# Kernel tuning notes

Hardware: AMD Instinct MI355X
Metric: run time of the kernel (lower is better)

Reference implementation:

```python
import jax, jax.numpy as jnp
import numpy as np

NUM_HEADS = 8
NUM_POINTS = 4


def _grid_sample_bilinear(img, grid, H, W):
    """torch F.grid_sample(mode='bilinear', padding='zeros', align_corners=False).
    img:  [B, H, W, D]   grid: [B, S, 2] with (x, y) in [-1, 1].
    Returns [B, S, D].
    """
    gx, gy = grid[..., 0], grid[..., 1]
    # align_corners=False pixel mapping
    x = ((gx + 1.0) * W - 1.0) * 0.5
    y = ((gy + 1.0) * H - 1.0) * 0.5
    x0 = jnp.floor(x)
    y0 = jnp.floor(y)
    wx1 = x - x0
    wy1 = y - y0
    x0i = x0.astype(jnp.int32)
    y0i = y0.astype(jnp.int32)
    img_flat = img.reshape(img.shape[0], H * W, img.shape[-1])  # [B, N, D]

    def corner(xi, yi, w):
        valid = (xi >= 0) & (xi < W) & (yi >= 0) & (yi < H)  # zeros padding
        idx = jnp.clip(yi, 0, H - 1) * W + jnp.clip(xi, 0, W - 1)  # [B, S]
        v = jnp.take_along_axis(img_flat, idx[..., None], axis=1)  # [B, S, D]
        return v * (w * valid.astype(img.dtype))[..., None]

    out = corner(x0i, y0i, (1.0 - wx1) * (1.0 - wy1))
    out += corner(x0i + 1, y0i, wx1 * (1.0 - wy1))
    out += corner(x0i, y0i + 1, (1.0 - wx1) * wy1)
    out += corner(x0i + 1, y0i + 1, wx1 * wy1)
    return out


def setup_inputs() -> dict:
    key = jax.random.key(0)
    ks = jax.random.split(key, 12)
    B, Q, D = 4, 1024, 256
    H, W = 128, 128
    nh, npts = NUM_HEADS, NUM_POINTS
    f32 = jnp.float32
    return {
        "query": jax.random.normal(ks[0], (B, Q, D), f32),
        "reference_points": jax.random.uniform(ks[1], (B, Q, 2), f32),
        "value": jax.random.normal(ks[2], (B, H * W, D), f32),
        "W_off": jax.random.normal(ks[3], (D, nh * npts * 2), f32) * 0.02,
        "b_off": jax.random.normal(ks[4], (nh * npts * 2,), f32) * 0.02,
        "W_attn": jax.random.normal(ks[5], (D, nh * npts), f32) * 0.02,
        "b_attn": jax.random.normal(ks[6], (nh * npts,), f32) * 0.02,
        "W_v": jax.random.normal(ks[7], (D, D), f32) * (D ** -0.5),
        "b_v": jnp.zeros((D,), f32),
        "W_out": jax.random.normal(ks[8], (nh * D, D), f32) * ((nh * D) ** -0.5),
        "b_out": jnp.zeros((D,), f32),
        "H": H,
        "W": W,
    }


def reference(query, reference_points, value, W_off, b_off, W_attn, b_attn,
              W_v, b_v, W_out, b_out, H, W):
    B, Q, D = query.shape
    nh, npts = NUM_HEADS, NUM_POINTS
    # learned offsets and per-point attention weights
    offsets = (query @ W_off + b_off).reshape(B, Q, nh, npts, 2)
    attn = jax.nn.softmax((query @ W_attn + b_attn).reshape(B, Q, nh, npts), axis=-1)
    # sampling locations in [-1, 1]
    locs = reference_points[:, :, None, None, :] + offsets * 0.1
    locs = jnp.clip(locs, 0.0, 1.0) * 2.0 - 1.0
    # value projection -> 2D feature map [B, H, W, D]
    img = (value @ W_v + b_v).reshape(B, H, W, D)
    # sample all heads/points at once
    grid = locs.reshape(B, Q * nh * npts, 2)
    sampled = _grid_sample_bilinear(img, grid, H, W).reshape(B, Q, nh, npts, D)
    # weighted reduce over points, concat heads
    weighted = jnp.einsum("bqhpd,bqhp->bqhd", sampled, attn)
    out = weighted.reshape(B, Q, nh * D) @ W_out + b_out
    return out
```

## Files before the change

kernel.cpp:

```cpp
#include <hip/hip_runtime.h>
#include <hip/hip_bf16.h>
#include <math.h>

constexpr int B  = 4;
constexpr int Q  = 1024;
constexpr int D  = 256;
constexpr int NH = 8;
constexpr int NP = 4;
constexpr int H  = 128;
constexpr int W  = 128;
constexpr int HW = H * W;
constexpr int KAUG = 2112;

typedef short   bf16x8  __attribute__((ext_vector_type(8)));
typedef float   f32x4   __attribute__((ext_vector_type(4)));
typedef short   short4v __attribute__((ext_vector_type(4)));
typedef unsigned short ushort8v __attribute__((ext_vector_type(8)));

__device__ inline unsigned short f2bf(float f) {
    union { float f; unsigned u; } v; v.f = f;
    unsigned r = v.u + 0x7fff + ((v.u >> 16) & 1);
    return (unsigned short)(r >> 16);
}
__device__ inline float bf2f(unsigned short s) {
    union { unsigned u; float f; } v; v.u = ((unsigned)s) << 16;
    return v.f;
}

__device__ inline void async16(const void* g, void* l) {
    __builtin_amdgcn_global_load_lds(
        (const __attribute__((address_space(1))) unsigned*)g,
        (__attribute__((address_space(3))) unsigned*)l, 16, 0, 0);
}

constexpr int R1_SG   = 0;
constexpr int R1_WC   = R1_SG + 128;
constexpr int R1_BV   = R1_WC + 128;
constexpr int R1_CONV = R1_BV + (D * 64) / 256;
constexpr int R1_END  = R1_CONV + (B * HW * D) / 4096;

__global__ __launch_bounds__(256)
void k_stage1(const float* __restrict__ value,
              const float* __restrict__ query,
              const float* __restrict__ W_off,  const float* __restrict__ b_off,
              const float* __restrict__ W_attn, const float* __restrict__ b_attn,
              const float* __restrict__ b_v,    const float* __restrict__ W_out,
              const float* __restrict__ W_v,
              unsigned short* __restrict__ val_bf,
              float* __restrict__ raw,
              unsigned short* __restrict__ WcT) {
    __shared__ __align__(16) unsigned char smemraw[16384];
    const int blk = blockIdx.x;
    const int tid = threadIdx.x;

    if (blk < R1_WC) {
        const int m0 = (blk >> 1) * 64;
        const int n0 = (blk & 1) * 64;
        float (*As)[68] = (float (*)[68])smemraw;
        float (*Bs)[68] = As + 16;
        const int tx = tid & 15, ty = tid >> 4;
        const int arow = tid >> 2, akg = (tid & 3) * 4;
        const int brow = tid >> 4, bcol = (tid & 15) * 4;

        float acc[4][4] = {};
        for (int k0 = 0; k0 < D; k0 += 16) {
            const float4 av = *(const float4*)&query[(size_t)(m0 + arow) * D + k0 + akg];
            const int kr = k0 + brow;
            const int j  = n0 + bcol;
            float4 bv;
            if (j < 64)      bv = *(const float4*)&W_off[kr * 64 + j];
            else if (j < 96) bv = *(const float4*)&W_attn[kr * 32 + (j - 64)];
            else             bv = (float4){0.f, 0.f, 0.f, 0.f};
            __syncthreads();
            As[akg + 0][arow] = av.x;
            As[akg + 1][arow] = av.y;
            As[akg + 2][arow] = av.z;
            As[akg + 3][arow] = av.w;
            *(float4*)&Bs[brow][bcol] = bv;
            __syncthreads();
            #pragma unroll
            for (int kk = 0; kk < 16; ++kk) {
                const float4 a = *(const float4*)&As[kk][ty * 4];
                const float4 b = *(const float4*)&Bs[kk][tx * 4];
                acc[0][0] += a.x * b.x; acc[0][1] += a.x * b.y; acc[0][2] += a.x * b.z; acc[0][3] += a.x * b.w;
                acc[1][0] += a.y * b.x; acc[1][1] += a.y * b.y; acc[1][2] += a.y * b.z; acc[1][3] += a.y * b.w;
                acc[2][0] += a.z * b.x; acc[2][1] += a.z * b.y; acc[2][2] += a.z * b.z; acc[2][3] += a.z * b.w;
                acc[3][0] += a.w * b.x; acc[3][1] += a.w * b.y; acc[3][2] += a.w * b.z; acc[3][3] += a.w * b.w;
            }
        }
        float bb[4];
        #pragma unroll
        for (int c = 0; c < 4; ++c) {
            const int col = n0 + tx * 4 + c;
            bb[c] = (col < 64) ? b_off[col] : ((col < 96) ? b_attn[col - 64] : 0.0f);
        }
        #pragma unroll
        for (int i = 0; i < 4; ++i) {
            const int m = m0 + ty * 4 + i;
            float4 r;
            r.x = acc[i][0] + bb[0];
            r.y = acc[i][1] + bb[1];
            r.z = acc[i][2] + bb[2];
            r.w = acc[i][3] + bb[3];
            *(float4*)&raw[(size_t)m * 128 + n0 + tx * 4] = r;
        }
    } else if (blk < R1_BV) {
        const int blkr = blk - R1_WC;
        const int z  = blkr >> 4;
        const int m0 = ((blkr >> 2) & 3) * 64;
        const int n0 = (blkr & 3) * 64;
        unsigned short* As = (unsigned short*)smemraw;
        unsigned short* Bs = As + 4096;
        const int lane = tid & 63;
        const int w    = tid >> 6;
        const int wm   = w >> 1, wn = w & 1;

        int aoff[2][2], boff[2][2];
        #pragma unroll
        for (int i = 0; i < 2; ++i)
            #pragma unroll
            for (int kk = 0; kk < 2; ++kk) {
                const int ar = wm * 32 + i * 16 + (lane & 15);
                aoff[i][kk] = ar * 64 + ((((lane >> 4) + kk * 4) ^ (ar & 7)) * 8);
                const int br = wn * 32 + i * 16 + (lane & 15);
                boff[i][kk] = br * 64 + ((((lane >> 4) + kk * 4) ^ (br & 7)) * 8);
            }

        f32x4 acc[2][2];
        #pragma unroll
        for (int i = 0; i < 2; ++i)
            #pragma unroll
            for (int j = 0; j < 2; ++j) acc[i][j] = (f32x4){0.f, 0.f, 0.f, 0.f};

        for (int it = 0; it < 4; ++it) {
            const int k0 = it * 64;
            __syncthreads();
            #pragma unroll
            for (int s = 0; s < 2; ++s) {
                const int cc = tid + s * 256;
                const int r = cc >> 3, c = cc & 7;
                const float4 v0 = *(const float4*)&W_v[(size_t)(m0 + r) * D + k0 + c * 8];
                const float4 v1 = *(const float4*)&W_v[(size_t)(m0 + r) * D + k0 + c * 8 + 4];
                ushort8v o;
                o[0] = f2bf(v0.x); o[1] = f2bf(v0.y); o[2] = f2bf(v0.z); o[3] = f2bf(v0.w);
                o[4] = f2bf(v1.x); o[5] = f2bf(v1.y); o[6] = f2bf(v1.z); o[7] = f2bf(v1.w);
                *(ushort8v*)&As[r * 64 + ((c ^ (r & 7)) * 8)] = o;
            }
            {
                const int n = tid & 63, kseg = tid >> 6;
                float vj[16];
                #pragma unroll
                for (int j = 0; j < 16; ++j)
                    vj[j] = W_out[(size_t)(z * 256 + k0 + kseg * 16 + j) * D + n0 + n];
                #pragma unroll
                for (int jj = 0; jj < 2; ++jj) {
                    ushort8v o;
                    #pragma unroll
                    for (int q = 0; q < 8; ++q) o[q] = f2bf(vj[jj * 8 + q]);
                    const int c = kseg * 2 + jj;
                    *(ushort8v*)&Bs[n * 64 + ((c ^ (n & 7)) * 8)] = o;
                }
            }
            __syncthreads();
            bf16x8 af[2][2], bfv[2][2];
            #pragma unroll
            for (int i = 0; i < 2; ++i)
                #pragma unroll
                for (int kk = 0; kk < 2; ++kk) {
                    af[i][kk]  = *(const bf16x8*)&As[aoff[i][kk]];
                    bfv[i][kk] = *(const bf16x8*)&Bs[boff[i][kk]];
                }
            #pragma unroll
            for (int i = 0; i < 2; ++i)
                #pragma unroll
                for (int j = 0; j < 2; ++j)
                    #pragma unroll
                    for (int kk = 0; kk < 2; ++kk)
                        acc[i][j] = __builtin_amdgcn_mfma_f32_16x16x32_bf16(
                            af[i][kk], bfv[j][kk], acc[i][j], 0, 0, 0);
        }

        const int colb = n0 + wn * 32 + (lane & 15);
        const int rowb = m0 + wm * 32 + (lane >> 4) * 4;
        const int ocol = z * 256;
        #pragma unroll
        for (int j = 0; j < 2; ++j) {
            const int col = colb + j * 16;
            #pragma unroll
            for (int i = 0; i < 2; ++i)
                #pragma unroll
                for (int r = 0; r < 4; ++r)
                    WcT[(size_t)col * KAUG + ocol + rowb + i * 16 + r] =
                        f2bf(acc[i][j][r]);
        }
    } else if (blk < R1_CONV) {
        const int t = (blk - R1_BV) * 256 + tid;
        const int n = t >> 6, c = t & 63;
        float v = 0.0f;
        if (c < 8) {
            #pragma unroll 8
            for (int j = 0; j < D; ++j)
                v += b_v[j] * W_out[((size_t)c * D + j) * D + n];
        }
        WcT[(size_t)n * KAUG + 2048 + c] = f2bf(v);
    } else {
        const int base = (blk - R1_CONV) * 4096;
        #pragma unroll
        for (int s = 0; s < 4; ++s) {
            const int i = base + s * 1024 + tid * 4;
            const float4 v = *(const float4*)&value[i];
            short4v o;
            o.x = (short)f2bf(v.x); o.y = (short)f2bf(v.y);
            o.z = (short)f2bf(v.z); o.w = (short)f2bf(v.w);
            *(short4v*)&val_bf[i] = o;
        }
    }
}

__global__ __launch_bounds__(256)
void k_stage2(const unsigned short* __restrict__ val,
              const float* __restrict__ raw,
              const float* __restrict__ refpts,
              unsigned short* __restrict__ sv) {
    const int bq   = blockIdx.x;
    const int b    = bq >> 10;
    const int tid  = threadIdx.x;
    const int lane = tid & 63;
    const int w    = tid >> 6;

    __shared__ float s_raw[128];
    __shared__ int   s_off[128];
    __shared__ float s_wgt[128];

    if (tid < 128) s_raw[tid] = raw[(size_t)bq * 128 + tid];
    __syncthreads();

    if (tid < NH * NP) {
        const int h = tid >> 2;
        float m = -1e30f;
        #pragma unroll
        for (int p = 0; p < NP; ++p) m = fmaxf(m, s_raw[64 + h * 4 + p]);
        float s = 0.0f;
        #pragma unroll
        for (int p = 0; p < NP; ++p) s += __expf(s_raw[64 + h * 4 + p] - m);
        const float a = __expf(s_raw[64 + tid] - m) / s;

        const float refx = refpts[(size_t)bq * 2 + 0];
        const float refy = refpts[(size_t)bq * 2 + 1];
        const float gx = fminf(fmaxf(refx + s_raw[tid * 2 + 0] * 0.1f, 0.0f), 1.0f) * 2.0f - 1.0f;
        const float gy = fminf(fmaxf(refy + s_raw[tid * 2 + 1] * 0.1f, 0.0f), 1.0f) * 2.0f - 1.0f;
        const float x  = ((gx + 1.0f) * (float)W - 1.0f) * 0.5f;
        const float y  = ((gy + 1.0f) * (float)H - 1.0f) * 0.5f;
        const float x0f = floorf(x), y0f = floorf(y);
        const float wx1 = x - x0f,  wy1 = y - y0f;
        const float wx0 = 1.0f - wx1, wy0 = 1.0f - wy1;
        const int x0 = (int)x0f, y0 = (int)y0f;
        const int x1 = x0 + 1,  y1 = y0 + 1;
        const float vx0 = (x0 >= 0 && x0 < W) ? 1.0f : 0.0f;
        const float vx1 = (x1 >= 0 && x1 < W) ? 1.0f : 0.0f;
        const float vy0 = (y0 >= 0 && y0 < H) ? 1.0f : 0.0f;
        const float vy1 = (y1 >= 0 && y1 < H) ? 1.0f : 0.0f;
        const int xc0 = min(max(x0, 0), W - 1);
        const int xc1 = min(max(x1, 0), W - 1);
        const int yc0 = min(max(y0, 0), H - 1);
        const int yc1 = min(max(y1, 0), H - 1);
        s_off[tid * 4 + 0] = yc0 * W + xc0;
        s_off[tid * 4 + 1] = yc0 * W + xc1;
        s_off[tid * 4 + 2] = yc1 * W + xc0;
        s_off[tid * 4 + 3] = yc1 * W + xc1;
        s_wgt[tid * 4 + 0] = a * wx0 * wy0 * vx0 * vy0;
        s_wgt[tid * 4 + 1] = a * wx1 * wy0 * vx1 * vy0;
        s_wgt[tid * 4 + 2] = a * wx0 * wy1 * vx0 * vy1;
        s_wgt[tid * 4 + 3] = a * wx1 * wy1 * vx1 * vy1;
    }
    __syncthreads();

    if (tid < 8) {
        float S = 0.0f;
        #pragma unroll
        for (int c = 0; c < 16; ++c) S += s_wgt[tid * 16 + c];
        sv[(size_t)bq * KAUG + 2048 + tid] = f2bf(S);
    } else if (tid < 64) {
        sv[(size_t)bq * KAUG + 2048 + tid] = 0;
    }

    const int half = lane >> 5;
    const int l5   = lane & 31;
    const unsigned short* ib = val + (size_t)b * HW * D + l5 * 8;

    ushort8v vb[16];
    float    wg[16];
    #pragma unroll
    for (int j = 0; j < 16; ++j) {
        const int flat = w * 32 + j * 2 + half;
        wg[j] = s_wgt[flat];
        vb[j] = *(const ushort8v*)(ib + (size_t)s_off[flat] * D);
    }

    float acc[2][8] = {};
    #pragma unroll
    for (int j = 0; j < 16; ++j) {
        const int g = j >> 3;
        #pragma unroll
        for (int k = 0; k < 8; ++k)
            acc[g][k] += wg[j] * bf2f(vb[j][k]);
    }

    #pragma unroll
    for (int hh = 0; hh < 2; ++hh) {
        float comb[8];
        #pragma unroll
        for (int k = 0; k < 8; ++k)
            comb[k] = acc[hh][k] + __shfl_xor(acc[hh][k], 32, 64);
        if (half == 0) {
            const int h = w * 2 + hh;
            ushort8v o;
            #pragma unroll
            for (int k = 0; k < 8; ++k) o[k] = f2bf(comb[k]);
            *(ushort8v*)&sv[(size_t)bq * KAUG + h * D + l5 * 8] = o;
        }
    }
}

__global__ __launch_bounds__(256)
void k_stage3(const unsigned short* __restrict__ sv,
              const unsigned short* __restrict__ WcT,
              const float* __restrict__ b_out,
              float* __restrict__ out) {
    __shared__ __align__(16) unsigned short lds[12288];

    const int tid  = threadIdx.x;
    const int lane = tid & 63;
    const int w    = tid >> 6;
    const int m0 = blockIdx.x * 32, n0 = blockIdx.y * 64;

    const int srow = w * 8 + (lane >> 3);
    const int schk = (lane & 7) ^ (lane >> 3);
    const unsigned short* ag  = sv  + (size_t)(m0 + srow)      * KAUG + schk * 8;
    const unsigned short* bg0 = WcT + (size_t)(n0 + srow)      * KAUG + schk * 8;
    const unsigned short* bg1 = WcT + (size_t)(n0 + srow + 32) * KAUG + schk * 8;
    const int la = w * 512 + lane * 8;
    const int lb = la;

    int aoff[2][2], boff[2];
    #pragma unroll
    for (int i = 0; i < 2; ++i)
        #pragma unroll
        for (int kk = 0; kk < 2; ++kk) {
            const int ar = i * 16 + (lane & 15);
            aoff[i][kk] = ar * 64 + ((((lane >> 4) + kk * 4) ^ (ar & 7)) * 8);
        }
    #pragma unroll
    for (int kk = 0; kk < 2; ++kk) {
        const int br = w * 16 + (lane & 15);
        boff[kk] = br * 64 + ((((lane >> 4) + kk * 4) ^ (br & 7)) * 8);
    }

    f32x4 acc[2];
    acc[0] = (f32x4){0.f, 0.f, 0.f, 0.f};
    acc[1] = (f32x4){0.f, 0.f, 0.f, 0.f};

    async16(ag,  &lds[0 + la]);
    async16(bg0, &lds[2048 + lb]);
    async16(bg1, &lds[2048 + 2048 + lb]);

    const int niter = KAUG >> 6;
    for (int it = 0; it < niter; ++it) {
        __syncthreads();
        const int cur = (it & 1) * 6144;
        if (it + 1 < niter) {
            const int nxt = 6144 - cur;
            const int ko  = (it + 1) * 64;
            async16(ag + ko,  &lds[nxt + la]);
            async16(bg0 + ko, &lds[nxt + 2048 + lb]);
            async16(bg1 + ko, &lds[nxt + 4096 + lb]);
        }
        bf16x8 af[2][2], bfv[2];
        #pragma unroll
        for (int kk = 0; kk < 2; ++kk) {
            bfv[kk] = *(const bf16x8*)&lds[cur + 2048 + boff[kk]];
            #pragma unroll
            for (int i = 0; i < 2; ++i)
                af[i][kk] = *(const bf16x8*)&lds[cur + aoff[i][kk]];
        }
        #pragma unroll
        for (int i = 0; i < 2; ++i)
            #pragma unroll
            for (int kk = 0; kk < 2; ++kk)
                acc[i] = __builtin_amdgcn_mfma_f32_16x16x32_bf16(
                    af[i][kk], bfv[kk], acc[i], 0, 0, 0);
    }

    const int col = n0 + w * 16 + (lane & 15);
    const float bb = b_out[col];
    const int rowb = m0 + (lane >> 4) * 4;
    #pragma unroll
    for (int i = 0; i < 2; ++i)
        #pragma unroll
        for (int r = 0; r < 4; ++r)
            out[(size_t)(rowb + i * 16 + r) * D + col] = acc[i][r] + bb;
}

extern "C" void kernel_launch(void* const* d_in, const int* in_sizes, int n_in,
                              void* d_out, int out_size, void* d_ws, size_t ws_size,
                              hipStream_t stream) {
    const float* query  = (const float*)d_in[0];
    const float* refpts = (const float*)d_in[1];
    const float* value  = (const float*)d_in[2];
    const float* W_off  = (const float*)d_in[3];
    const float* b_off  = (const float*)d_in[4];
    const float* W_attn = (const float*)d_in[5];
    const float* b_attn = (const float*)d_in[6];
    const float* W_v    = (const float*)d_in[7];
    const float* b_v    = (const float*)d_in[8];
    const float* W_out  = (const float*)d_in[9];
    const float* b_out  = (const float*)d_in[10];
    float* out = (float*)d_out;

    char* wsb = (char*)d_ws;
    unsigned short* val_bf = (unsigned short*)(wsb);
    unsigned short* sv     = (unsigned short*)(wsb + 33554432);
    unsigned short* WcT    = (unsigned short*)(wsb + 50855936);
    float*          raw    = (float*)(wsb + 51937280);

    k_stage1<<<R1_END, 256, 0, stream>>>(value, query, W_off, b_off,
                                         W_attn, b_attn, b_v, W_out, W_v,
                                         val_bf, raw, WcT);

    k_stage2<<<B * Q, 256, 0, stream>>>(val_bf, raw, refpts, sv);

    {
        dim3 grid((B * Q) / 32, D / 64);
        k_stage3<<<grid, 256, 0, stream>>>(sv, WcT, b_out, out);
    }
}
```

Before: 172.7 us.

## Reorder sampling blocks by spatial bucket of reference points for cache locality

Adds extra blocks to stage1 that bucket each batch's queries into a 16x16 spatial grid by reference point, using a shared-memory counting sort to build a permutation. Stage2 then processes queries in this spatially sorted order, so blocks running at the same time gather from nearby regions of the bf16 value map. The aim is better L2/MALL reuse of the gathered value rows. The cost is a small sort pass and one extra indirection per block.

```diff
diff --git a/kernel.cpp b/kernel.cpp
--- a/kernel.cpp
+++ b/kernel.cpp
@@ -38,6 +38,7 @@
 constexpr int R1_BV   = R1_WC + 128;
 constexpr int R1_CONV = R1_BV + (D * 64) / 256;
 constexpr int R1_END  = R1_CONV + (B * HW * D) / 4096;
+constexpr int R1_TOT  = R1_END + B;
 
 __global__ __launch_bounds__(256)
 void k_stage1(const float* __restrict__ value,
@@ -46,9 +47,11 @@
               const float* __restrict__ W_attn, const float* __restrict__ b_attn,
               const float* __restrict__ b_v,    const float* __restrict__ W_out,
               const float* __restrict__ W_v,
+              const float* __restrict__ refpts,
               unsigned short* __restrict__ val_bf,
               float* __restrict__ raw,
-              unsigned short* __restrict__ WcT) {
+              unsigned short* __restrict__ WcT,
+              int* __restrict__ perm) {
     __shared__ __align__(16) unsigned char smemraw[16384];
     const int blk = blockIdx.x;
     const int tid = threadIdx.x;
@@ -203,7 +206,7 @@
                 v += b_v[j] * W_out[((size_t)c * D + j) * D + n];
         }
         WcT[(size_t)n * KAUG + 2048 + c] = f2bf(v);
-    } else {
+    } else if (blk < R1_END) {
         const int base = (blk - R1_CONV) * 4096;
         #pragma unroll
         for (int s = 0; s < 4; ++s) {
@@ -214,6 +217,39 @@
             o.z = (short)f2bf(v.z); o.w = (short)f2bf(v.w);
             *(short4v*)&val_bf[i] = o;
         }
+    } else {
+        const int b = blk - R1_END;
+        __shared__ int cnt[256];
+        __shared__ int scr[256];
+        cnt[tid] = 0;
+        __syncthreads();
+        int bkt_l[4];
+        #pragma unroll
+        for (int s = 0; s < 4; ++s) {
+            const int q = s * 256 + tid;
+            const float2 rp = ((const float2*)refpts)[(size_t)b * 1024 + q];
+            int bx = (int)(rp.x * 16.0f); bx = min(max(bx, 0), 15);
+            int by = (int)(rp.y * 16.0f); by = min(max(by, 0), 15);
+            bkt_l[s] = by * 16 + bx;
+            atomicAdd(&cnt[bkt_l[s]], 1);
+        }
+        __syncthreads();
+        const int run = cnt[tid];
+        int incl = run;
+        for (int off = 1; off < 256; off <<= 1) {
+            scr[tid] = incl;
+            __syncthreads();
+            if (tid >= off) incl += scr[tid - off];
+            __syncthreads();
+        }
+        cnt[tid] = incl - run;
+        __syncthreads();
+        #pragma unroll
+        for (int s = 0; s < 4; ++s) {
+            const int q = s * 256 + tid;
+            const int pos = atomicAdd(&cnt[bkt_l[s]], 1);
+            perm[b * 1024 + pos] = q;
+        }
     }
 }
 
@@ -221,9 +257,11 @@
 void k_stage2(const unsigned short* __restrict__ val,
               const float* __restrict__ raw,
               const float* __restrict__ refpts,
+              const int* __restrict__ perm,
               unsigned short* __restrict__ sv) {
-    const int bq   = blockIdx.x;
-    const int b    = bq >> 10;
+    const int bi   = blockIdx.x;
+    const int b    = bi >> 10;
+    const int bq   = (b << 10) | perm[bi];
     const int tid  = threadIdx.x;
     const int lane = tid & 63;
     const int w    = tid >> 6;
@@ -422,12 +460,13 @@
     unsigned short* sv     = (unsigned short*)(wsb + 33554432);
     unsigned short* WcT    = (unsigned short*)(wsb + 50855936);
     float*          raw    = (float*)(wsb + 51937280);
-
-    k_stage1<<<R1_END, 256, 0, stream>>>(value, query, W_off, b_off,
+    int*            perm   = (int*)(wsb + 54034432);
+
+    k_stage1<<<R1_TOT, 256, 0, stream>>>(value, query, W_off, b_off,
                                          W_attn, b_attn, b_v, W_out, W_v,
-                                         val_bf, raw, WcT);
-
-    k_stage2<<<B * Q, 256, 0, stream>>>(val_bf, raw, refpts, sv);
+                                         refpts, val_bf, raw, WcT, perm);
+
+    k_stage2<<<B * Q, 256, 0, stream>>>(val_bf, raw, refpts, perm, sv);
 
     {
         dim3 grid((B * Q) / 32, D / 64);
```

New measurement: 169.9 us. No clear change (-1.6%).
